# Optimization experiments

Measured on AMD Instinct MI355X. Metric: run time of the kernel, lower is better.

Reference implementation:

```python
import jax, jax.numpy as jnp
import numpy as np
from jax import lax


def _binarize(w):
    # XNOR-style sign binarization: sign(w) with sign(0) -> +1
    return jnp.where(w >= 0, 1.0, -1.0).astype(w.dtype)


def setup_inputs() -> dict:
    key = jax.random.key(0)
    kx, kw = jax.random.split(key)
    X = jax.random.normal(kx, (32, 256, 56, 56), dtype=jnp.float32)   # NCHW
    W = jax.random.normal(kw, (256, 256, 3, 3), dtype=jnp.float32)    # OIHW
    return {"X": X, "W": W}


def reference(X, W):
    Wb = _binarize(W)
    # F.conv2d default: padding=0 (VALID), stride=1
    out = lax.conv_general_dilated(
        X, Wb,
        window_strides=(1, 1),
        padding="VALID",
        dimension_numbers=("NCHW", "OIHW", "NCHW"),
    )
    return out  # [32, 256, 54, 54]
```

## Files before the change

kernel.cpp:

```cpp
#include <hip/hip_runtime.h>
#include <stdint.h>

typedef float f32x4 __attribute__((ext_vector_type(4)));
typedef __bf16 bf16x8 __attribute__((ext_vector_type(8)));
typedef unsigned short u16x8 __attribute__((ext_vector_type(8)));

#define NIMG 32
#define CIN  256
#define HIN  56
#define WIN  56
#define HWIN 3136
#define COUT 256
#define HOUT 54
#define WOUT 54
#define HWOUT 2916
#define NPOS 93312

#define XT_BYTES   ((size_t)NIMG*HWIN*CIN*2)
#define WT_OFF     (XT_BYTES + 8192)
#define WT_BYTES   ((size_t)9*8*256*32*2)
#define WS_NEED    (WT_OFF + WT_BYTES)

static __device__ __forceinline__ unsigned short f2bf(float f) {
    union { float f; uint32_t u; } v; v.f = f;
    return (unsigned short)((v.u + 0x7FFFu + ((v.u >> 16) & 1u)) >> 16);
}

static __device__ __forceinline__ void gload16(const void* g, void* l) {
    __builtin_amdgcn_global_load_lds(
        (const __attribute__((address_space(1))) void*)g,
        (__attribute__((address_space(3))) void*)l, 16, 0, 0);
}

__global__ void wxform(const float* __restrict__ W, unsigned short* __restrict__ Wt) {
    int idx = blockIdx.x * 256 + threadIdx.x;
    int cb = idx & 31;
    int o  = (idx >> 5) & 255;
    int cc = (idx >> 13) & 7;
    int k  = idx >> 16;
    int c  = cc * 32 + cb;
    float w = W[(size_t)(o * 256 + c) * 9 + k];
    Wt[idx] = (w >= 0.0f) ? (unsigned short)0x3F80 : (unsigned short)0xBF80;
}

__global__ void xxform(const float* __restrict__ X, unsigned short* __restrict__ Xt) {
    __shared__ float tile[32][65];
    int bid = blockIdx.x;
    int hwc = bid % 49;
    int cc  = (bid / 49) & 7;
    int n   = bid / (49 * 8);
    int hw0 = hwc * 64;
    int c0  = cc * 32;
    int t = threadIdx.x;
    {
        int c = t >> 3;
        int w = (t & 7) * 8;
        const float* src = X + (size_t)(n * CIN + c0 + c) * HWIN + hw0 + w;
        float4 a = *(const float4*)src;
        float4 b = *(const float4*)(src + 4);
        tile[c][w + 0] = a.x; tile[c][w + 1] = a.y; tile[c][w + 2] = a.z; tile[c][w + 3] = a.w;
        tile[c][w + 4] = b.x; tile[c][w + 5] = b.y; tile[c][w + 6] = b.z; tile[c][w + 7] = b.w;
    }
    __syncthreads();
    {
        int w  = t >> 2;
        int cb = (t & 3) * 8;
        u16x8 v;
        #pragma unroll
        for (int j = 0; j < 8; ++j) v[j] = f2bf(tile[cb + j][w]);
        *(u16x8*)(Xt + (size_t)(n * HWIN + hw0 + w) * 256 + c0 + cb) = v;
    }
}

__global__ __launch_bounds__(128, 2)
void bconv_gemm(const unsigned short* __restrict__ Xt,
                const unsigned short* __restrict__ Wt,
                float* __restrict__ out) {
    __shared__ __align__(16) unsigned short lds[4096 + 2048];
    const int t    = threadIdx.x;
    const int wid  = t >> 6;
    const int lane = t & 63;
    const int l15  = lane & 15;
    const int lg   = lane >> 4;
    const uint32_t P0 = blockIdx.x * 64u;
    const int o0 = blockIdx.y * 128;

    const int cb16 = (t & 3) * 8;
    uint32_t base0[2];
    #pragma unroll
    for (int r = 0; r < 2; ++r) {
        uint32_t P  = P0 + (t >> 2) + r * 32;
        uint32_t n  = P / (uint32_t)HWOUT;
        uint32_t rm = P - n * HWOUT;
        uint32_t ph = rm / 54u;
        uint32_t pw = rm - ph * 54u;
        base0[r] = n * HWIN + ph * 56u + pw;
    }

    f32x4 acc[4][4];
    #pragma unroll
    for (int m = 0; m < 4; ++m)
        #pragma unroll
        for (int nn = 0; nn < 4; ++nn)
            acc[m][nn] = (f32x4){0.f, 0.f, 0.f, 0.f};

    uint32_t aoff[4], boff[4];
    #pragma unroll
    for (int m = 0; m < 4; ++m)  aoff[m] = (uint32_t)((wid * 64 + m * 16 + l15) * 32 + lg * 8);
    #pragma unroll
    for (int nn = 0; nn < 4; ++nn) boff[nn] = (uint32_t)(4096 + (nn * 16 + l15) * 32 + lg * 8);

    for (int kh = 0; kh < 3; ++kh) {
        for (int c0 = 0; c0 < 8; ++c0) {
            #pragma unroll
            for (int kw = 0; kw < 3; ++kw) {
                const int k9 = kh * 3 + kw;
                const unsigned short* aG = Wt + (size_t)(k9 * 8 + c0) * 8192 + o0 * 32 + t * 8;
                #pragma unroll
                for (int r = 0; r < 4; ++r)
                    gload16(aG + r * 1024, (unsigned short*)lds + r * 1024 + t * 8);
                const uint32_t khw = (uint32_t)(kh * 56 + kw);
                #pragma unroll
                for (int r = 0; r < 2; ++r) {
                    const unsigned short* bG = Xt + ((size_t)(base0[r] + khw)) * 256 + c0 * 32 + cb16;
                    gload16(bG, (unsigned short*)lds + 4096 + r * 1024 + t * 8);
                }
                __syncthreads();
                bf16x8 af[4], bfr[4];
                #pragma unroll
                for (int m = 0; m < 4; ++m)
                    af[m] = __builtin_bit_cast(bf16x8, *(const u16x8*)(lds + aoff[m]));
                #pragma unroll
                for (int nn = 0; nn < 4; ++nn)
                    bfr[nn] = __builtin_bit_cast(bf16x8, *(const u16x8*)(lds + boff[nn]));
                #pragma unroll
                for (int m = 0; m < 4; ++m)
                    #pragma unroll
                    for (int nn = 0; nn < 4; ++nn)
                        acc[m][nn] = __builtin_amdgcn_mfma_f32_16x16x32_bf16(
                            af[m], bfr[nn], acc[m][nn], 0, 0, 0);
                __syncthreads();
            }
        }
    }

    #pragma unroll
    for (int nn = 0; nn < 4; ++nn) {
        uint32_t P  = P0 + nn * 16 + l15;
        uint32_t n  = P / (uint32_t)HWOUT;
        uint32_t rm = P - n * HWOUT;
        float* obase = out + (size_t)(n * 256u + o0 + wid * 64) * HWOUT + rm;
        #pragma unroll
        for (int m = 0; m < 4; ++m)
            #pragma unroll
            for (int r = 0; r < 4; ++r)
                obase[(size_t)(m * 16 + lg * 4 + r) * HWOUT] = acc[m][nn][r];
    }
}

__global__ void bconv_fallback(const float* __restrict__ X, const float* __restrict__ W,
                               float* __restrict__ out) {
    size_t idx = (size_t)blockIdx.x * 256 + threadIdx.x;
    int ow = (int)(idx % 54);
    int oh = (int)((idx / 54) % 54);
    int o  = (int)((idx / 2916) % 256);
    int n  = (int)(idx / 746496);
    float s = 0.f;
    for (int c = 0; c < 256; ++c) {
        const float* xr = X + ((size_t)(n * 256 + c) * 56 + oh) * 56 + ow;
        const float* wr = W + (size_t)(o * 256 + c) * 9;
        #pragma unroll
        for (int kh = 0; kh < 3; ++kh)
            #pragma unroll
            for (int kw = 0; kw < 3; ++kw) {
                float w = wr[kh * 3 + kw];
                float x = xr[kh * 56 + kw];
                s += (w >= 0.f) ? x : -x;
            }
    }
    out[idx] = s;
}

extern "C" void kernel_launch(void* const* d_in, const int* in_sizes, int n_in,
                              void* d_out, int out_size, void* d_ws, size_t ws_size,
                              hipStream_t stream) {
    const float* X = (const float*)d_in[0];
    const float* W = (const float*)d_in[1];
    float* out = (float*)d_out;

    if (ws_size < WS_NEED) {
        bconv_fallback<<<93312, 256, 0, stream>>>(X, W, out);
        return;
    }
    unsigned short* Xt = (unsigned short*)d_ws;
    unsigned short* Wt = (unsigned short*)((char*)d_ws + WT_OFF);

    wxform<<<2304, 256, 0, stream>>>(W, Wt);
    xxform<<<12544, 256, 0, stream>>>(X, Xt);

    dim3 grid(1458, 2);
    bconv_gemm<<<grid, 128, 0, stream>>>(Xt, Wt, out);
}
```

Baseline: 171.1 us.

## Rewrite implicit-GEMM conv as 256x128 tile with triple-buffered async LDS pipeline

The GEMM kernel is replaced with a 512-thread block that covers all 256 output channels and 128 positions, and the K step grows from 32 to 64 channels. The weight layout changes to match, and LDS uses an XOR swizzle. Three buffered stages are loaded asynchronously with explicit vmcnt waits and a single barrier per phase, plus MFMA priority raising and inline ds_read_b128. The aim is to hide global-load latency, cut barrier count, and remove the duplicate input loads across output-channel blocks. In exchange it needs 144KB of LDS per block, depends on precise waitcnt bookkeeping, and uses a fixed grid of 729 blocks.

```diff
diff --git a/kernel.cpp b/kernel.cpp
--- a/kernel.cpp
+++ b/kernel.cpp
@@ -7,18 +7,14 @@
 
 #define NIMG 32
 #define CIN  256
-#define HIN  56
-#define WIN  56
 #define HWIN 3136
 #define COUT 256
-#define HOUT 54
-#define WOUT 54
 #define HWOUT 2916
 #define NPOS 93312
 
 #define XT_BYTES   ((size_t)NIMG*HWIN*CIN*2)
 #define WT_OFF     (XT_BYTES + 8192)
-#define WT_BYTES   ((size_t)9*8*256*32*2)
+#define WT_BYTES   ((size_t)36*256*64*2)
 #define WS_NEED    (WT_OFF + WT_BYTES)
 
 static __device__ __forceinline__ unsigned short f2bf(float f) {
@@ -32,14 +28,36 @@
         (__attribute__((address_space(3))) void*)l, 16, 0, 0);
 }
 
+static __device__ __forceinline__ uint32_t lds_a(const void* p) {
+    return (uint32_t)(uintptr_t)(__attribute__((address_space(3))) const void*)p;
+}
+
+static __device__ __forceinline__ u16x8 ldsr(uint32_t addr) {
+    u16x8 r;
+    asm volatile("ds_read_b128 %0, %1" : "=v"(r) : "v"(addr));
+    return r;
+}
+
+#define BAR()   __builtin_amdgcn_s_barrier()
+#define LGKM0() do { asm volatile("s_waitcnt lgkmcnt(0)" ::: "memory"); \
+                     __builtin_amdgcn_sched_barrier(0); } while (0)
+#define VM12()  asm volatile("s_waitcnt vmcnt(12)" ::: "memory")
+#define VM6()   asm volatile("s_waitcnt vmcnt(6)" ::: "memory")
+#define VM0()   asm volatile("s_waitcnt vmcnt(0)" ::: "memory")
+#define PRIO1() __builtin_amdgcn_s_setprio(1)
+#define PRIO0() __builtin_amdgcn_s_setprio(0)
+
+#define MF(a_, b_, c_) __builtin_amdgcn_mfma_f32_16x16x32_bf16( \
+    __builtin_bit_cast(bf16x8, a_), __builtin_bit_cast(bf16x8, b_), c_, 0, 0, 0)
+
 __global__ void wxform(const float* __restrict__ W, unsigned short* __restrict__ Wt) {
     int idx = blockIdx.x * 256 + threadIdx.x;
-    int cb = idx & 31;
-    int o  = (idx >> 5) & 255;
-    int cc = (idx >> 13) & 7;
-    int k  = idx >> 16;
-    int c  = cc * 32 + cb;
-    float w = W[(size_t)(o * 256 + c) * 9 + k];
+    int c6 = idx & 63;
+    int o  = (idx >> 6) & 255;
+    int cc = (idx >> 14) & 3;
+    int k9 = idx >> 16;
+    int c = cc * 64 + c6;
+    float w = W[(size_t)(o * 256 + c) * 9 + k9];
     Wt[idx] = (w >= 0.0f) ? (unsigned short)0x3F80 : (unsigned short)0xBF80;
 }
 
@@ -72,89 +90,130 @@
     }
 }
 
-__global__ __launch_bounds__(128, 2)
+__global__ __launch_bounds__(512, 2)
 void bconv_gemm(const unsigned short* __restrict__ Xt,
                 const unsigned short* __restrict__ Wt,
                 float* __restrict__ out) {
-    __shared__ __align__(16) unsigned short lds[4096 + 2048];
+    __shared__ __align__(16) char smem[147456];
+
     const int t    = threadIdx.x;
     const int wid  = t >> 6;
     const int lane = t & 63;
     const int l15  = lane & 15;
     const int lg   = lane >> 4;
-    const uint32_t P0 = blockIdx.x * 64u;
-    const int o0 = blockIdx.y * 128;
-
-    const int cb16 = (t & 3) * 8;
-    uint32_t base0[2];
+    const int wr   = wid >> 2;
+    const int wc   = wid & 3;
+    const uint32_t P0 = blockIdx.x * 128u;
+
+    const uint32_t colxB = (uint32_t)(((t & 7) ^ ((t >> 3) & 7)) << 4);
+    const uint32_t rowt  = (uint32_t)(t >> 3);
+
+    const char* pA0 = (const char*)Wt + rowt * 128 + colxB;
+
+    const char* bB[2];
     #pragma unroll
     for (int r = 0; r < 2; ++r) {
-        uint32_t P  = P0 + (t >> 2) + r * 32;
-        uint32_t n  = P / (uint32_t)HWOUT;
-        uint32_t rm = P - n * HWOUT;
+        uint32_t pos = P0 + (uint32_t)(r * 64) + rowt;
+        uint32_t ni = pos / (uint32_t)HWOUT;
+        uint32_t rm = pos - ni * HWOUT;
         uint32_t ph = rm / 54u;
         uint32_t pw = rm - ph * 54u;
-        base0[r] = n * HWIN + ph * 56u + pw;
-    }
-
-    f32x4 acc[4][4];
-    #pragma unroll
-    for (int m = 0; m < 4; ++m)
-        #pragma unroll
-        for (int nn = 0; nn < 4; ++nn)
-            acc[m][nn] = (f32x4){0.f, 0.f, 0.f, 0.f};
-
-    uint32_t aoff[4], boff[4];
-    #pragma unroll
-    for (int m = 0; m < 4; ++m)  aoff[m] = (uint32_t)((wid * 64 + m * 16 + l15) * 32 + lg * 8);
-    #pragma unroll
-    for (int nn = 0; nn < 4; ++nn) boff[nn] = (uint32_t)(4096 + (nn * 16 + l15) * 32 + lg * 8);
-
-    for (int kh = 0; kh < 3; ++kh) {
-        for (int c0 = 0; c0 < 8; ++c0) {
-            #pragma unroll
-            for (int kw = 0; kw < 3; ++kw) {
-                const int k9 = kh * 3 + kw;
-                const unsigned short* aG = Wt + (size_t)(k9 * 8 + c0) * 8192 + o0 * 32 + t * 8;
-                #pragma unroll
-                for (int r = 0; r < 4; ++r)
-                    gload16(aG + r * 1024, (unsigned short*)lds + r * 1024 + t * 8);
-                const uint32_t khw = (uint32_t)(kh * 56 + kw);
-                #pragma unroll
-                for (int r = 0; r < 2; ++r) {
-                    const unsigned short* bG = Xt + ((size_t)(base0[r] + khw)) * 256 + c0 * 32 + cb16;
-                    gload16(bG, (unsigned short*)lds + 4096 + r * 1024 + t * 8);
-                }
-                __syncthreads();
-                bf16x8 af[4], bfr[4];
-                #pragma unroll
-                for (int m = 0; m < 4; ++m)
-                    af[m] = __builtin_bit_cast(bf16x8, *(const u16x8*)(lds + aoff[m]));
-                #pragma unroll
-                for (int nn = 0; nn < 4; ++nn)
-                    bfr[nn] = __builtin_bit_cast(bf16x8, *(const u16x8*)(lds + boff[nn]));
-                #pragma unroll
-                for (int m = 0; m < 4; ++m)
-                    #pragma unroll
-                    for (int nn = 0; nn < 4; ++nn)
-                        acc[m][nn] = __builtin_amdgcn_mfma_f32_16x16x32_bf16(
-                            af[m], bfr[nn], acc[m][nn], 0, 0, 0);
-                __syncthreads();
-            }
-        }
-    }
-
-    #pragma unroll
-    for (int nn = 0; nn < 4; ++nn) {
-        uint32_t P  = P0 + nn * 16 + l15;
-        uint32_t n  = P / (uint32_t)HWOUT;
-        uint32_t rm = P - n * HWOUT;
-        float* obase = out + (size_t)(n * 256u + o0 + wid * 64) * HWOUT + rm;
-        #pragma unroll
-        for (int m = 0; m < 4; ++m)
+        bB[r] = (const char*)Xt + (size_t)(ni * HWIN + ph * 56u + pw) * 512 + colxB;
+    }
+
+    const uint32_t x7  = (uint32_t)(l15 & 7);
+    const uint32_t ck0 = ((((uint32_t)lg) ^ x7) << 4);
+    const uint32_t ck1 = (((4u | (uint32_t)lg) ^ x7) << 4);
+    uint32_t arow[8], brow[2];
+    #pragma unroll
+    for (int m = 0; m < 8; ++m) arow[m] = (uint32_t)(wr * 128 + m * 16 + l15) * 128u;
+    #pragma unroll
+    for (int n = 0; n < 2; ++n) brow[n] = 32768u + (uint32_t)(wc * 32 + n * 16 + l15) * 128u;
+
+    const uint32_t L0 = lds_a(smem);
+
+    f32x4 acc[8][2];
+    #pragma unroll
+    for (int m = 0; m < 8; ++m)
+        #pragma unroll
+        for (int n = 0; n < 2; ++n)
+            acc[m][n] = (f32x4){0.f, 0.f, 0.f, 0.f};
+
+    uint32_t cc3 = 3, k3 = 0, koff = 384;
+
+    auto STAGE = [&](uint32_t off, int ktp3, uint32_t kof) {
+        const char* p = pA0 + (size_t)ktp3 * 32768u;
+        #pragma unroll
+        for (int r = 0; r < 4; ++r)
+            gload16(p + r * 8192, smem + off + r * 8192 + (size_t)t * 16);
+        #pragma unroll
+        for (int r = 0; r < 2; ++r)
+            gload16(bB[r] + kof, smem + off + 32768 + r * 8192 + (size_t)t * 16);
+    };
+
+    STAGE(0u, 0, 0u);
+    STAGE(49152u, 1, 128u);
+    STAGE(98304u, 2, 256u);
+    VM12();
+    BAR();
+
+    auto PHASE = [&](uint32_t off, int kt, int mode) {
+        u16x8 A0[8], A1[8], F0[2], F1[2];
+        const uint32_t base = L0 + off;
+        #pragma unroll
+        for (int m = 0; m < 8; ++m) {
+            A0[m] = ldsr(base + arow[m] + ck0);
+            A1[m] = ldsr(base + arow[m] + ck1);
+        }
+        #pragma unroll
+        for (int n = 0; n < 2; ++n) {
+            F0[n] = ldsr(base + brow[n] + ck0);
+            F1[n] = ldsr(base + brow[n] + ck1);
+        }
+        if (mode == 2) { VM0(); } else { VM6(); }
+        LGKM0();
+        BAR();
+        if (mode == 0) {
+            STAGE(off, kt + 3, koff);
+            if (cc3 == 3) { cc3 = 0; koff += ((k3 == 2) ? 54u : 1u) * 512u - 384u; k3 = (k3 == 2) ? 0u : k3 + 1u; }
+            else          { cc3++; koff += 128u; }
+        }
+        PRIO1();
+        #pragma unroll
+        for (int m = 0; m < 8; ++m) {
+            acc[m][0] = MF(A0[m], F0[0], acc[m][0]);
+            acc[m][1] = MF(A0[m], F0[1], acc[m][1]);
+        }
+        #pragma unroll
+        for (int m = 0; m < 8; ++m) {
+            acc[m][0] = MF(A1[m], F1[0], acc[m][0]);
+            acc[m][1] = MF(A1[m], F1[1], acc[m][1]);
+        }
+        PRIO0();
+    };
+
+    int kt = 0;
+    for (int g = 0; g < 11; ++g) {
+        PHASE(0u, kt, 0); ++kt;
+        PHASE(49152u, kt, 0); ++kt;
+        PHASE(98304u, kt, 0); ++kt;
+    }
+    PHASE(0u, 33, 1);
+    PHASE(49152u, 34, 2);
+    PHASE(98304u, 35, 2);
+
+    #pragma unroll
+    for (int n = 0; n < 2; ++n) {
+        uint32_t P = P0 + (uint32_t)(wc * 32 + n * 16 + l15);
+        uint32_t ni = P / (uint32_t)HWOUT;
+        uint32_t rm = P - ni * HWOUT;
+        float* ob_ = out + (size_t)(ni * 256u) * HWOUT + rm;
+        #pragma unroll
+        for (int m = 0; m < 8; ++m) {
             #pragma unroll
             for (int r = 0; r < 4; ++r)
-                obase[(size_t)(m * 16 + lg * 4 + r) * HWOUT] = acc[m][nn][r];
+                ob_[(size_t)(wr * 128 + m * 16 + lg * 4 + r) * HWOUT] = acc[m][n][r];
+        }
     }
 }
 
@@ -198,6 +257,5 @@
     wxform<<<2304, 256, 0, stream>>>(W, Wt);
     xxform<<<12544, 256, 0, stream>>>(X, Xt);
 
-    dim3 grid(1458, 2);
-    bconv_gemm<<<grid, 128, 0, stream>>>(Xt, Wt, out);
-}
+    bconv_gemm<<<729, 512, 0, stream>>>(Xt, Wt, out);
+}
```

Result: faster. 145.9 us (-14.8%).
